# Optimization experiments

Hardware: AMD Instinct MI355X
Metric: run time of the kernel (lower is better)

The kernel has to match this reference:

```python
import jax, jax.numpy as jnp
import numpy as np
from jax import lax

B, S, T = 512, 64, 32
E, H = 512, 1024
VIN, VOUT = 128, 128


def gru_cell(x, h, W_ih, W_hh, b_ih, b_hh):
    # PyTorch GRU cell: gates ordered (r, z, n)
    gi = x @ W_ih.T + b_ih           # [B, 3*Hh]
    gh = h @ W_hh.T + b_hh           # [B, 3*Hh]
    i_r, i_z, i_n = jnp.split(gi, 3, axis=-1)
    h_r, h_z, h_n = jnp.split(gh, 3, axis=-1)
    r = jax.nn.sigmoid(i_r + h_r)
    z = jax.nn.sigmoid(i_z + h_z)
    n = jnp.tanh(i_n + r * h_n)
    return (1.0 - z) * n + z * h


def setup_inputs() -> dict:
    key = jax.random.key(0)
    ks = jax.random.split(key, 18)
    g = lambda k, shp: (jax.random.normal(k, shp, jnp.float32) * 0.05)
    return {
        "src": jax.random.randint(ks[0], (B, S), 0, VIN),
        "tgt": jax.random.randint(ks[1], (B, T), 0, VOUT),
        "enc_emb": g(ks[2], (VIN, E)),
        "dec_emb": g(ks[3], (VOUT, E)),
        "W_ih_f": g(ks[4], (3 * H, E)), "W_hh_f": g(ks[5], (3 * H, H)),
        "b_ih_f": g(ks[6], (3 * H,)), "b_hh_f": g(ks[7], (3 * H,)),
        "W_ih_b": g(ks[8], (3 * H, E)), "W_hh_b": g(ks[9], (3 * H, H)),
        "b_ih_b": g(ks[10], (3 * H,)), "b_hh_b": g(ks[11], (3 * H,)),
        "W_ih_d": g(ks[12], (3 * 2 * H, E)), "W_hh_d": g(ks[13], (3 * 2 * H, 2 * H)),
        "b_ih_d": g(ks[14], (3 * 2 * H,)), "b_hh_d": g(ks[15], (3 * 2 * H,)),
        "W_fc": g(ks[16], (VOUT, 2 * H)), "b_fc": g(ks[17], (VOUT,)),
    }


def reference(src, tgt, enc_emb, dec_emb,
              W_ih_f, W_hh_f, b_ih_f, b_hh_f,
              W_ih_b, W_hh_b, b_ih_b, b_hh_b,
              W_ih_d, W_hh_d, b_ih_d, b_hh_d,
              W_fc, b_fc):
    batch = src.shape[0]
    x = enc_emb[src]                         # [B, S, E]
    x_t = jnp.swapaxes(x, 0, 1)              # [S, B, E]

    def enc_scan(xs, W_ih, W_hh, b_ih, b_hh):
        h0 = jnp.zeros((batch, H), dtype=xs.dtype)
        def step(h, xt):
            h2 = gru_cell(xt, h, W_ih, W_hh, b_ih, b_hh)
            return h2, None
        hT, _ = lax.scan(step, h0, xs)
        return hT                             # final hidden [B, H]

    h_fwd = enc_scan(x_t, W_ih_f, W_hh_f, b_ih_f, b_hh_f)
    h_bwd = enc_scan(x_t[::-1], W_ih_b, W_hh_b, b_ih_b, b_hh_b)
    h = jnp.concatenate([h_fwd, h_bwd], axis=-1)   # [B, 2H] = torch.cat((h[-2], h[-1]), 1)

    tok0 = tgt[:, 0]                          # <sos> tokens

    def dec_step(carry, _):
        hh, tok = carry
        xt = dec_emb[tok]                     # [B, E]
        hh = gru_cell(xt, hh, W_ih_d, W_hh_d, b_ih_d, b_hh_d)
        logits = hh @ W_fc.T + b_fc           # [B, VOUT]
        nxt = jnp.argmax(logits, axis=-1)     # greedy feedback (teacher_forcing_ratio=0)
        return (hh, nxt), logits

    (_, _), logits = lax.scan(dec_step, (h, tok0), None, length=tgt.shape[1] - 1)
    return jnp.swapaxes(logits, 0, 1)         # [B, T-1, VOUT]
```

## Files before the change

### kernel.cpp

```cpp
#include <hip/hip_runtime.h>
#include <math.h>

#define B 512
#define S 64
#define T 32
#define E 512
#define H 1024
#define VOUTD 128
#define H2 (2*H)
#define H3 (3*H)
#define H6 (6*H)

typedef unsigned short ushortT;
typedef unsigned int uintT;
typedef __attribute__((ext_vector_type(8))) short short8;
typedef __attribute__((ext_vector_type(4))) float floatx4;

__device__ __forceinline__ float sigmoidf_(float x) { return 1.0f / (1.0f + expf(-x)); }

__device__ __forceinline__ uintT pack_hi2(float a, float b) {
    return (__float_as_uint(a) >> 16) | (__float_as_uint(b) & 0xFFFF0000u);
}
__device__ __forceinline__ uintT pack_lo2(float a, float b) {
    uintT ua = __float_as_uint(a), ub = __float_as_uint(b);
    uintT la = __float_as_uint(a - __uint_as_float(ua & 0xFFFF0000u)) >> 16;
    uintT lb = __float_as_uint(b - __uint_as_float(ub & 0xFFFF0000u)) >> 16;
    return la | (lb << 16);
}

__global__ __launch_bounds__(256) void zero16(uint4* __restrict__ p, int n)
{
    int i = blockIdx.x * 256 + threadIdx.x;
    if (i < n) p[i] = make_uint4(0u, 0u, 0u, 0u);
}

__global__ __launch_bounds__(256) void swizzle_w(
    const float* __restrict__ W, ushortT* __restrict__ out, int njShift, int kShift)
{
    int idx = blockIdx.x * 256 + threadIdx.x;
    int total = 3 << (njShift + kShift);
    if (idx >= total) return;
    int wrow = idx >> kShift;
    int k8 = idx & ((1 << kShift) - 1);
    int k = k8 << 3;
    int K = 8 << kShift;
    const float* s = W + (size_t)wrow * K + k;
    float4 f0 = *(const float4*)s;
    float4 f1 = *(const float4*)(s + 4);
    int g = wrow >> njShift;
    int j = wrow & ((1 << njShift) - 1);
    int jb = j >> 4, jl = j & 15;
    int c = k >> 5, kq = (k >> 3) & 3;
    int laneA = jl + 16 * kq;
    int ncK = K >> 5;
    size_t base = (((size_t)(jb * ncK + c) * 3 + g) * 2) * 512 + (size_t)laneA * 8;
    uint4 hv = make_uint4(pack_hi2(f0.x, f0.y), pack_hi2(f0.z, f0.w),
                          pack_hi2(f1.x, f1.y), pack_hi2(f1.z, f1.w));
    uint4 lv = make_uint4(pack_lo2(f0.x, f0.y), pack_lo2(f0.z, f0.w),
                          pack_lo2(f1.x, f1.y), pack_lo2(f1.z, f1.w));
    *(uint4*)(out + base) = hv;
    *(uint4*)(out + base + 512) = lv;
}

__global__ __launch_bounds__(256) void fused_step_enc(
    const ushortT* __restrict__ Afr,
    const ushortT* __restrict__ WfrF, const ushortT* __restrict__ WfrB,
    const float* __restrict__ giTabF, const float* __restrict__ giTabB,
    const int* __restrict__ src, int s,
    const float* __restrict__ bhF, const float* __restrict__ bhB,
    float* __restrict__ h, ushortT* __restrict__ AfrOut)
{
    __shared__ ushortT sB[2][24 * 512];
    __shared__ int sTok[64];
    const int t = threadIdx.x, lane = t & 63, w = t >> 6;
    const int bid = blockIdx.x;
    const int xcd = bid & 7, q = bid >> 3;
    const int jg = xcd + 8 * (q & 3);
    const int mb = q >> 2;
    const int j0 = jg * 32, m0 = mb * 64;
    const bool bwd = (m0 >= B);
    const ushortT* Wfr = bwd ? WfrB : WfrF;
    const float* giTab = bwd ? giTabB : giTabF;
    const float* bh = bwd ? bhB : bhF;
    const int NCK = 32, NIT = 16;

    if (t < 64) {
        int b = (m0 + t) & (B - 1);
        sTok[t] = src[b * S + (bwd ? (S - 1 - s) : s)];
    }

    const int wr = w >> 1, wc = w & 1;
    const ushortT* aP = Afr + (size_t)((m0 >> 4) + wr * 2) * (NCK * 1024) + lane * 8;

    const ushortT* gWb[3];
    int lds0[3], lds1[3];
#pragma unroll
    for (int k = 0; k < 3; ++k) {
        int f = w * 3 + k;
        int jbLoc = f / 6, rem = f % 6;
        gWb[k] = Wfr + (size_t)(jg * 2 + jbLoc) * (NCK * 3072) + rem * 512 + lane * 8;
        lds0[k] = f * 512 + lane * 8;
        lds1[k] = (12 + f) * 512 + lane * 8;
    }
    const int rb0 = wc * 3072 + lane * 8;

    floatx4 acc[2][3];
#pragma unroll
    for (int mi = 0; mi < 2; ++mi)
#pragma unroll
        for (int g = 0; g < 3; ++g) acc[mi][g] = (floatx4){0.f, 0.f, 0.f, 0.f};

    uint4 st0[3], st1[3];
#pragma unroll
    for (int k = 0; k < 3; ++k) {
        st0[k] = *(const uint4*)(gWb[k]);
        st1[k] = *(const uint4*)(gWb[k] + 3072);
    }
#pragma unroll
    for (int k = 0; k < 3; ++k) {
        *(uint4*)&sB[0][lds0[k]] = st0[k];
        *(uint4*)&sB[0][lds1[k]] = st1[k];
    }
    __syncthreads();

    short8 an00 = *(const short8*)(aP);
    short8 an01 = *(const short8*)(aP + 512);
    short8 an10 = *(const short8*)(aP + NCK * 1024);
    short8 an11 = *(const short8*)(aP + NCK * 1024 + 512);

    int pb = 0;
    for (int it = 0; it < NIT; ++it) {
        if (it + 1 < NIT) {
            int cb = (it + 1) * 2;
#pragma unroll
            for (int k = 0; k < 3; ++k) {
                st0[k] = *(const uint4*)(gWb[k] + (size_t)cb * 3072);
                st1[k] = *(const uint4*)(gWb[k] + (size_t)(cb + 1) * 3072);
            }
        }
        const ushortT* bp = &sB[pb][0];
        {
            short8 a00 = an00, a01 = an01, a10 = an10, a11 = an11;
            int cn = 2 * it + 1;
            an00 = *(const short8*)(aP + (size_t)cn * 1024);
            an01 = *(const short8*)(aP + (size_t)cn * 1024 + 512);
            an10 = *(const short8*)(aP + (size_t)cn * 1024 + NCK * 1024);
            an11 = *(const short8*)(aP + (size_t)cn * 1024 + NCK * 1024 + 512);
#pragma unroll
            for (int g = 0; g < 3; ++g) {
                short8 bhf = *(const short8*)&bp[rb0 + g * 1024];
                short8 blf = *(const short8*)&bp[rb0 + g * 1024 + 512];
                acc[0][g] = __builtin_amdgcn_mfma_f32_16x16x32_bf16(a00, bhf, acc[0][g], 0, 0, 0);
                acc[0][g] = __builtin_amdgcn_mfma_f32_16x16x32_bf16(a00, blf, acc[0][g], 0, 0, 0);
                acc[0][g] = __builtin_amdgcn_mfma_f32_16x16x32_bf16(a01, bhf, acc[0][g], 0, 0, 0);
                acc[1][g] = __builtin_amdgcn_mfma_f32_16x16x32_bf16(a10, bhf, acc[1][g], 0, 0, 0);
                acc[1][g] = __builtin_amdgcn_mfma_f32_16x16x32_bf16(a10, blf, acc[1][g], 0, 0, 0);
                acc[1][g] = __builtin_amdgcn_mfma_f32_16x16x32_bf16(a11, bhf, acc[1][g], 0, 0, 0);
            }
        }
        {
            short8 a00 = an00, a01 = an01, a10 = an10, a11 = an11;
            int cn = 2 * it + 2; if (cn >= NCK) cn = NCK - 1;
            an00 = *(const short8*)(aP + (size_t)cn * 1024);
            an01 = *(const short8*)(aP + (size_t)cn * 1024 + 512);
            an10 = *(const short8*)(aP + (size_t)cn * 1024 + NCK * 1024);
            an11 = *(const short8*)(aP + (size_t)cn * 1024 + NCK * 1024 + 512);
#pragma unroll
            for (int g = 0; g < 3; ++g) {
                short8 bhf = *(const short8*)&bp[12 * 512 + rb0 + g * 1024];
                short8 blf = *(const short8*)&bp[12 * 512 + rb0 + g * 1024 + 512];
                acc[0][g] = __builtin_amdgcn_mfma_f32_16x16x32_bf16(a00, bhf, acc[0][g], 0, 0, 0);
                acc[0][g] = __builtin_amdgcn_mfma_f32_16x16x32_bf16(a00, blf, acc[0][g], 0, 0, 0);
                acc[0][g] = __builtin_amdgcn_mfma_f32_16x16x32_bf16(a01, bhf, acc[0][g], 0, 0, 0);
                acc[1][g] = __builtin_amdgcn_mfma_f32_16x16x32_bf16(a10, bhf, acc[1][g], 0, 0, 0);
                acc[1][g] = __builtin_amdgcn_mfma_f32_16x16x32_bf16(a10, blf, acc[1][g], 0, 0, 0);
                acc[1][g] = __builtin_amdgcn_mfma_f32_16x16x32_bf16(a11, bhf, acc[1][g], 0, 0, 0);
            }
        }
        if (it + 1 < NIT) {
#pragma unroll
            for (int k = 0; k < 3; ++k) {
                *(uint4*)&sB[pb ^ 1][lds0[k]] = st0[k];
                *(uint4*)&sB[pb ^ 1][lds1[k]] = st1[k];
            }
            __syncthreads();
            pb ^= 1;
        }
    }

    const int colj = j0 + wc * 16 + (lane & 15);
    const float bR = bh[colj], bZ = bh[H + colj], bN = bh[2 * H + colj];
    const int rloc0 = wr * 32 + (lane >> 4) * 4;
    const int cA = colj >> 5;
    const int kqA = (colj >> 3) & 3;
    const int eA = colj & 7;
#pragma unroll
    for (int mi = 0; mi < 2; ++mi) {
#pragma unroll
        for (int r = 0; r < 4; ++r) {
            const int rloc = rloc0 + mi * 16 + r;
            const int row = m0 + rloc;
            const float* gi = giTab + (size_t)sTok[rloc] * H3;
            float ghr = acc[mi][0][r] + bR;
            float ghz = acc[mi][1][r] + bZ;
            float ghn = acc[mi][2][r] + bN;
            float rr = sigmoidf_(gi[colj] + ghr);
            float z  = sigmoidf_(gi[H + colj] + ghz);
            float n  = tanhf(gi[2 * H + colj] + rr * ghn);
            const size_t idx = (size_t)row * H + colj;
            float hnew = (1.0f - z) * n + z * h[idx];
            h[idx] = hnew;
            uintT u = __float_as_uint(hnew);
            size_t ao = (((size_t)(row >> 4) * 32 + cA) * 2) * 512
                      + (size_t)((row & 15) + 16 * kqA) * 8 + eA;
            AfrOut[ao] = (ushortT)(u >> 16);
            AfrOut[ao + 512] = (ushortT)(__float_as_uint(hnew - __uint_as_float(u & 0xFFFF0000u)) >> 16);
        }
    }
}

__global__ __launch_bounds__(256) void fused_step_dec(
    const ushortT* __restrict__ Afr, const ushortT* __restrict__ Wfr,
    const float* __restrict__ giTabD, const int* __restrict__ tok,
    const float* __restrict__ bhD,
    float* __restrict__ h, ushortT* __restrict__ AfrOut)
{
    __shared__ ushortT sB[2][24 * 512];
    __shared__ int sTok[64];
    const int t = threadIdx.x, lane = t & 63, w = t >> 6;
    const int bid = blockIdx.x;
    const int xcd = bid & 7, q = bid >> 3;
    const int jg = xcd + 8 * (q & 7);
    const int mb = q >> 3;
    const int j0 = jg * 32, m0 = mb * 64;
    const int NCK = 64, NIT = 32;

    if (t < 64) sTok[t] = tok[m0 + t];

    const int wr = w >> 1, wc = w & 1;
    const ushortT* aP = Afr + (size_t)((m0 >> 4) + wr * 2) * (NCK * 1024) + lane * 8;

    const ushortT* gWb[3];
    int lds0[3], lds1[3];
#pragma unroll
    for (int k = 0; k < 3; ++k) {
        int f = w * 3 + k;
        int jbLoc = f / 6, rem = f % 6;
        gWb[k] = Wfr + (size_t)(jg * 2 + jbLoc) * (NCK * 3072) + rem * 512 + lane * 8;
        lds0[k] = f * 512 + lane * 8;
        lds1[k] = (12 + f) * 512 + lane * 8;
    }
    const int rb0 = wc * 3072 + lane * 8;

    floatx4 acc[2][3];
#pragma unroll
    for (int mi = 0; mi < 2; ++mi)
#pragma unroll
        for (int g = 0; g < 3; ++g) acc[mi][g] = (floatx4){0.f, 0.f, 0.f, 0.f};

    uint4 st0[3], st1[3];
#pragma unroll
    for (int k = 0; k < 3; ++k) {
        st0[k] = *(const uint4*)(gWb[k]);
        st1[k] = *(const uint4*)(gWb[k] + 3072);
    }
#pragma unroll
    for (int k = 0; k < 3; ++k) {
        *(uint4*)&sB[0][lds0[k]] = st0[k];
        *(uint4*)&sB[0][lds1[k]] = st1[k];
    }
    __syncthreads();

    short8 an00 = *(const short8*)(aP);
    short8 an01 = *(const short8*)(aP + 512);
    short8 an10 = *(const short8*)(aP + NCK * 1024);
    short8 an11 = *(const short8*)(aP + NCK * 1024 + 512);

    int pb = 0;
    for (int it = 0; it < NIT; ++it) {
        if (it + 1 < NIT) {
            int cb = (it + 1) * 2;
#pragma unroll
            for (int k = 0; k < 3; ++k) {
                st0[k] = *(const uint4*)(gWb[k] + (size_t)cb * 3072);
                st1[k] = *(const uint4*)(gWb[k] + (size_t)(cb + 1) * 3072);
            }
        }
        const ushortT* bp = &sB[pb][0];
        {
            short8 a00 = an00, a01 = an01, a10 = an10, a11 = an11;
            int cn = 2 * it + 1;
            an00 = *(const short8*)(aP + (size_t)cn * 1024);
            an01 = *(const short8*)(aP + (size_t)cn * 1024 + 512);
            an10 = *(const short8*)(aP + (size_t)cn * 1024 + NCK * 1024);
            an11 = *(const short8*)(aP + (size_t)cn * 1024 + NCK * 1024 + 512);
#pragma unroll
            for (int g = 0; g < 3; ++g) {
                short8 bhf = *(const short8*)&bp[rb0 + g * 1024];
                short8 blf = *(const short8*)&bp[rb0 + g * 1024 + 512];
                acc[0][g] = __builtin_amdgcn_mfma_f32_16x16x32_bf16(a00, bhf, acc[0][g], 0, 0, 0);
                acc[0][g] = __builtin_amdgcn_mfma_f32_16x16x32_bf16(a00, blf, acc[0][g], 0, 0, 0);
                acc[0][g] = __builtin_amdgcn_mfma_f32_16x16x32_bf16(a01, bhf, acc[0][g], 0, 0, 0);
                acc[1][g] = __builtin_amdgcn_mfma_f32_16x16x32_bf16(a10, bhf, acc[1][g], 0, 0, 0);
                acc[1][g] = __builtin_amdgcn_mfma_f32_16x16x32_bf16(a10, blf, acc[1][g], 0, 0, 0);
                acc[1][g] = __builtin_amdgcn_mfma_f32_16x16x32_bf16(a11, bhf, acc[1][g], 0, 0, 0);
            }
        }
        {
            short8 a00 = an00, a01 = an01, a10 = an10, a11 = an11;
            int cn = 2 * it + 2; if (cn >= NCK) cn = NCK - 1;
            an00 = *(const short8*)(aP + (size_t)cn * 1024);
            an01 = *(const short8*)(aP + (size_t)cn * 1024 + 512);
            an10 = *(const short8*)(aP + (size_t)cn * 1024 + NCK * 1024);
            an11 = *(const short8*)(aP + (size_t)cn * 1024 + NCK * 1024 + 512);
#pragma unroll
            for (int g = 0; g < 3; ++g) {
                short8 bhf = *(const short8*)&bp[12 * 512 + rb0 + g * 1024];
                short8 blf = *(const short8*)&bp[12 * 512 + rb0 + g * 1024 + 512];
                acc[0][g] = __builtin_amdgcn_mfma_f32_16x16x32_bf16(a00, bhf, acc[0][g], 0, 0, 0);
                acc[0][g] = __builtin_amdgcn_mfma_f32_16x16x32_bf16(a00, blf, acc[0][g], 0, 0, 0);
                acc[0][g] = __builtin_amdgcn_mfma_f32_16x16x32_bf16(a01, bhf, acc[0][g], 0, 0, 0);
                acc[1][g] = __builtin_amdgcn_mfma_f32_16x16x32_bf16(a10, bhf, acc[1][g], 0, 0, 0);
                acc[1][g] = __builtin_amdgcn_mfma_f32_16x16x32_bf16(a10, blf, acc[1][g], 0, 0, 0);
                acc[1][g] = __builtin_amdgcn_mfma_f32_16x16x32_bf16(a11, bhf, acc[1][g], 0, 0, 0);
            }
        }
        if (it + 1 < NIT) {
#pragma unroll
            for (int k = 0; k < 3; ++k) {
                *(uint4*)&sB[pb ^ 1][lds0[k]] = st0[k];
                *(uint4*)&sB[pb ^ 1][lds1[k]] = st1[k];
            }
            __syncthreads();
            pb ^= 1;
        }
    }

    const int colj = j0 + wc * 16 + (lane & 15);
    const float bR = bhD[colj], bZ = bhD[H2 + colj], bN = bhD[2 * H2 + colj];
    const int rloc0 = wr * 32 + (lane >> 4) * 4;
    const int cA = colj >> 5;
    const int kqA = (colj >> 3) & 3;
    const int eA = colj & 7;
#pragma unroll
    for (int mi = 0; mi < 2; ++mi) {
#pragma unroll
        for (int r = 0; r < 4; ++r) {
            const int rloc = rloc0 + mi * 16 + r;
            const int row = m0 + rloc;
            const float* gi = giTabD + (size_t)sTok[rloc] * H6;
            float ghr = acc[mi][0][r] + bR;
            float ghz = acc[mi][1][r] + bZ;
            float ghn = acc[mi][2][r] + bN;
            float rr = sigmoidf_(gi[colj] + ghr);
            float z  = sigmoidf_(gi[H2 + colj] + ghz);
            float n  = tanhf(gi[2 * H2 + colj] + rr * ghn);
            const size_t idx = (size_t)row * H2 + colj;
            float hnew = (1.0f - z) * n + z * h[idx];
            h[idx] = hnew;
            uintT u = __float_as_uint(hnew);
            size_t ao = (((size_t)(row >> 4) * 64 + cA) * 2) * 512
                      + (size_t)((row & 15) + 16 * kqA) * 8 + eA;
            AfrOut[ao] = (ushortT)(u >> 16);
            AfrOut[ao + 512] = (ushortT)(__float_as_uint(hnew - __uint_as_float(u & 0xFFFF0000u)) >> 16);
        }
    }
}

__global__ __launch_bounds__(256) void init_hh_tok_split(
    const float* __restrict__ h_f, const float* __restrict__ h_b,
    const int* __restrict__ tgt, float* __restrict__ hh,
    ushortT* __restrict__ AfrD, int* __restrict__ tok)
{
    int i = blockIdx.x * blockDim.x + threadIdx.x;
    int b = i >> 11;
    int j = i & 2047;
    float v = (j < H) ? h_f[(size_t)b * H + j] : h_b[(size_t)b * H + (j - H)];
    hh[i] = v;
    uintT u = __float_as_uint(v);
    size_t ao = (((size_t)(b >> 4) * 64 + (j >> 5)) * 2) * 512
              + (size_t)((b & 15) + 16 * ((j >> 3) & 3)) * 8 + (j & 7);
    AfrD[ao] = (ushortT)(u >> 16);
    AfrD[ao + 512] = (ushortT)(__float_as_uint(v - __uint_as_float(u & 0xFFFF0000u)) >> 16);
    if (j == 0) tok[b] = tgt[b * T];
}

__global__ __launch_bounds__(256) void logits_argmax2(
    const float* __restrict__ hh, const float* __restrict__ W_fc,
    const float* __restrict__ b_fc, float* __restrict__ out,
    int* __restrict__ tok, int t)
{
    __shared__ float sh[2][H2];
    __shared__ float sred[2][2][128];
    __shared__ float sval[2][128];
    __shared__ int   sidx[2][128];
    const int tid = threadIdx.x;
    const int col = tid & 127;
    const int kh  = tid >> 7;
    const int b0  = blockIdx.x * 2;

    {
        const float4* srcp = (const float4*)(hh + (size_t)b0 * H2);
        float4* dst = (float4*)sh;
        for (int i = tid; i < 2 * H2 / 4; i += 256) dst[i] = srcp[i];
    }
    __syncthreads();

    const float* wrow = W_fc + (size_t)col * H2 + kh * (H2 / 2);
    const float* s0 = sh[0] + kh * (H2 / 2);
    const float* s1 = sh[1] + kh * (H2 / 2);
    float a0 = 0.f, a1 = 0.f;
#pragma unroll 8
    for (int k = 0; k < H2 / 2; k += 4) {
        float4 w4 = *(const float4*)(wrow + k);
        float4 h0 = *(const float4*)(s0 + k);
        float4 h1 = *(const float4*)(s1 + k);
        a0 += w4.x * h0.x + w4.y * h0.y + w4.z * h0.z + w4.w * h0.w;
        a1 += w4.x * h1.x + w4.y * h1.y + w4.z * h1.z + w4.w * h1.w;
    }
    sred[kh][0][col] = a0;
    sred[kh][1][col] = a1;
    __syncthreads();

    if (kh == 0) {
        float l0 = sred[0][0][col] + sred[1][0][col] + b_fc[col];
        float l1 = sred[0][1][col] + sred[1][1][col] + b_fc[col];
        out[(size_t)(b0 + 0) * ((T - 1) * VOUTD) + (size_t)t * VOUTD + col] = l0;
        out[(size_t)(b0 + 1) * ((T - 1) * VOUTD) + (size_t)t * VOUTD + col] = l1;
        sval[0][col] = l0; sidx[0][col] = col;
        sval[1][col] = l1; sidx[1][col] = col;
    }
    __syncthreads();

    const int r = tid >> 7, c = tid & 127;
    for (int off = 64; off > 0; off >>= 1) {
        if (c < off) {
            float ov = sval[r][c + off]; int oi = sidx[r][c + off];
            if (ov > sval[r][c] || (ov == sval[r][c] && oi < sidx[r][c])) {
                sval[r][c] = ov; sidx[r][c] = oi;
            }
        }
        __syncthreads();
    }
    if (tid < 2) tok[b0 + tid] = sidx[tid][0];
}

__global__ __launch_bounds__(256) void gemm_bias(
    const float* __restrict__ Abase,
    const int* __restrict__ idx, int idxStride, int idxOff, int lda,
    const float* __restrict__ W, const float* __restrict__ bias,
    float* __restrict__ C, int N, int K)
{
    __shared__ float As[16][68];
    __shared__ float Ws[16][68];
    const int t = threadIdx.x;
    const int m0 = blockIdx.y * 64, n0 = blockIdx.x * 64;
    const int lr = t >> 2, lc = (t & 3) << 2;
    const int tx = t & 15, ty = t >> 4;
    const int tn0 = tx << 2, tm0 = ty << 2;
    const int arow = m0 + lr;
    const float* Aptr = idx ? (Abase + (size_t)idx[arow * idxStride + idxOff] * lda)
                            : (Abase + (size_t)arow * lda);
    const float* Wptr = W + (size_t)(n0 + lr) * K;
    float acc[4][4] = {{0.f}};
    for (int k0 = 0; k0 < K; k0 += 16) {
        float4 a4 = *(const float4*)(Aptr + k0 + lc);
        float4 w4 = *(const float4*)(Wptr + k0 + lc);
        __syncthreads();
        As[lc+0][lr] = a4.x; As[lc+1][lr] = a4.y; As[lc+2][lr] = a4.z; As[lc+3][lr] = a4.w;
        Ws[lc+0][lr] = w4.x; Ws[lc+1][lr] = w4.y; Ws[lc+2][lr] = w4.z; Ws[lc+3][lr] = w4.w;
        __syncthreads();
#pragma unroll
        for (int kk = 0; kk < 16; ++kk) {
            float4 av = *(const float4*)&As[kk][tm0];
            float4 wv = *(const float4*)&Ws[kk][tn0];
            float am[4] = {av.x, av.y, av.z, av.w};
            float wn[4] = {wv.x, wv.y, wv.z, wv.w};
#pragma unroll
            for (int i = 0; i < 4; ++i)
#pragma unroll
                for (int j = 0; j < 4; ++j) acc[i][j] += am[i] * wn[j];
        }
    }
    const float b0 = bias[n0+tn0], b1 = bias[n0+tn0+1], b2 = bias[n0+tn0+2], b3 = bias[n0+tn0+3];
#pragma unroll
    for (int i = 0; i < 4; ++i) {
        float4 o = make_float4(acc[i][0]+b0, acc[i][1]+b1, acc[i][2]+b2, acc[i][3]+b3);
        *(float4*)(C + (size_t)(m0 + tm0 + i) * N + n0 + tn0) = o;
    }
}

__global__ __launch_bounds__(256) void gemm_enc(
    const float* __restrict__ Abase, int lda, int K,
    const int* __restrict__ srcIdx, int s,
    const float* __restrict__ W1, const float* __restrict__ bias1,
    const float* __restrict__ W2, const float* __restrict__ bias2,
    float* __restrict__ C, int N)
{
    __shared__ float As[16][68];
    __shared__ float Ws[16][68];
    const int t = threadIdx.x;
    const int m0 = blockIdx.y * 64, n0 = blockIdx.x * 64;
    const bool bwd = (m0 >= B);
    const float* W = bwd ? W2 : W1;
    const float* bias = bwd ? bias2 : bias1;
    const int lr = t >> 2, lc = (t & 3) << 2;
    const int tx = t & 15, ty = t >> 4;
    const int tn0 = tx << 2, tm0 = ty << 2;
    const int arow = m0 + lr;
    const float* Aptr;
    if (srcIdx) {
        int r = arow & (B - 1);
        int sidx = bwd ? (S - 1 - s) : s;
        Aptr = Abase + (size_t)srcIdx[r * S + sidx] * lda;
    } else Aptr = Abase + (size_t)arow * lda;
    const float* Wptr = W + (size_t)(n0 + lr) * K;
    float acc[4][4] = {{0.f}};
    for (int k0 = 0; k0 < K; k0 += 16) {
        float4 a4 = *(const float4*)(Aptr + k0 + lc);
        float4 w4 = *(const float4*)(Wptr + k0 + lc);
        __syncthreads();
        As[lc+0][lr] = a4.x; As[lc+1][lr] = a4.y; As[lc+2][lr] = a4.z; As[lc+3][lr] = a4.w;
        Ws[lc+0][lr] = w4.x; Ws[lc+1][lr] = w4.y; Ws[lc+2][lr] = w4.z; Ws[lc+3][lr] = w4.w;
        __syncthreads();
#pragma unroll
        for (int kk = 0; kk < 16; ++kk) {
            float4 av = *(const float4*)&As[kk][tm0];
            float4 wv = *(const float4*)&Ws[kk][tn0];
            float am[4] = {av.x, av.y, av.z, av.w};
            float wn[4] = {wv.x, wv.y, wv.z, wv.w};
#pragma unroll
            for (int i = 0; i < 4; ++i)
#pragma unroll
                for (int j = 0; j < 4; ++j) acc[i][j] += am[i] * wn[j];
        }
    }
    const float b0 = bias[n0+tn0], b1 = bias[n0+tn0+1], b2 = bias[n0+tn0+2], b3 = bias[n0+tn0+3];
#pragma unroll
    for (int i = 0; i < 4; ++i) {
        float4 o = make_float4(acc[i][0]+b0, acc[i][1]+b1, acc[i][2]+b2, acc[i][3]+b3);
        *(float4*)(C + (size_t)(m0 + tm0 + i) * N + n0 + tn0) = o;
    }
}

__global__ __launch_bounds__(256) void gru_gate(
    const float* __restrict__ gi, const float* __restrict__ gh,
    float* __restrict__ h, int Hd)
{
    int i = blockIdx.x * blockDim.x + threadIdx.x;
    int b = i / Hd, j = i - b * Hd;
    const float* gib = gi + (size_t)b * 3 * Hd;
    const float* ghb = gh + (size_t)b * 3 * Hd;
    float r = sigmoidf_(gib[j] + ghb[j]);
    float z = sigmoidf_(gib[Hd + j] + ghb[Hd + j]);
    float n = tanhf(gib[2 * Hd + j] + r * ghb[2 * Hd + j]);
    h[i] = (1.0f - z) * n + z * h[i];
}

__global__ __launch_bounds__(256) void init_hh_tok(
    const float* __restrict__ h_f, const float* __restrict__ h_b,
    const int* __restrict__ tgt, float* __restrict__ hh, int* __restrict__ tok)
{
    int i = blockIdx.x * blockDim.x + threadIdx.x;
    int b = i >> 11, j = i & 2047;
    hh[i] = (j < H) ? h_f[(size_t)b * H + j] : h_b[(size_t)b * H + (j - H)];
    if (j == 0) tok[b] = tgt[b * T];
}

extern "C" void kernel_launch(void* const* d_in, const int* in_sizes, int n_in,
                              void* d_out, int out_size, void* d_ws, size_t ws_size,
                              hipStream_t stream)
{
    const int*   src     = (const int*)d_in[0];
    const int*   tgt     = (const int*)d_in[1];
    const float* enc_emb = (const float*)d_in[2];
    const float* dec_emb = (const float*)d_in[3];
    const float* W_ih_f  = (const float*)d_in[4];
    const float* W_hh_f  = (const float*)d_in[5];
    const float* b_ih_f  = (const float*)d_in[6];
    const float* b_hh_f  = (const float*)d_in[7];
    const float* W_ih_b  = (const float*)d_in[8];
    const float* W_hh_b  = (const float*)d_in[9];
    const float* b_ih_b  = (const float*)d_in[10];
    const float* b_hh_b  = (const float*)d_in[11];
    const float* W_ih_d  = (const float*)d_in[12];
    const float* W_hh_d  = (const float*)d_in[13];
    const float* b_ih_d  = (const float*)d_in[14];
    const float* b_hh_d  = (const float*)d_in[15];
    const float* W_fc    = (const float*)d_in[16];
    const float* b_fc    = (const float*)d_in[17];
    float* out = (float*)d_out;

    char* base = (char*)d_ws;
    size_t off = 0;
    auto alloc = [&](size_t bytes) { char* p = base + off; off += (bytes + 255) & ~(size_t)255; return p; };

    float*   hE     = (float*)  alloc((size_t)2 * B * H * 4);
    ushortT* AfrEA  = (ushortT*)alloc((size_t)2 * B * H * 2 * 2);
    ushortT* AfrEB  = (ushortT*)alloc((size_t)2 * B * H * 2 * 2);
    float*   hh     = (float*)  alloc((size_t)B * H2 * 4);
    ushortT* AfrDA  = (ushortT*)alloc((size_t)B * H2 * 2 * 2);
    ushortT* AfrDB  = (ushortT*)alloc((size_t)B * H2 * 2 * 2);
    float*   giTabF = (float*)  alloc((size_t)VOUTD * H3 * 4);
    float*   giTabB = (float*)  alloc((size_t)VOUTD * H3 * 4);
    float*   giTabD = (float*)  alloc((size_t)VOUTD * H6 * 4);
    ushortT* WfrF   = (ushortT*)alloc((size_t)H3 * H * 2 * 2);
    ushortT* WfrB   = (ushortT*)alloc((size_t)H3 * H * 2 * 2);
    ushortT* WfrD   = (ushortT*)alloc((size_t)H6 * H2 * 2 * 2);
    int*     tok    = (int*)    alloc((size_t)B * 4);
    size_t required = off;

    dim3 blk(256);

    if (ws_size >= required) {
        {
            size_t zbytes = (size_t)2 * B * H * 4 + (size_t)2 * B * H * 4;
            int n16 = (int)(zbytes / 16);
            zero16<<<dim3((n16 + 255) / 256), blk, 0, stream>>>((uint4*)hE, n16);
        }
        swizzle_w<<<dim3((3 * H3 * H / (3 * 8) * 3 / 256) ? ((3 << 17) + 255) / 256 : 1), blk, 0, stream>>>(
            W_hh_f, WfrF, 10, 7);
        swizzle_w<<<dim3(((3 << 17) + 255) / 256), blk, 0, stream>>>(W_hh_b, WfrB, 10, 7);
        swizzle_w<<<dim3(((3 << 19) + 255) / 256), blk, 0, stream>>>(W_hh_d, WfrD, 11, 8);

        gemm_bias<<<dim3(H3 / 64, VOUTD / 64), blk, 0, stream>>>(
            enc_emb, nullptr, 0, 0, E, W_ih_f, b_ih_f, giTabF, H3, E);
        gemm_bias<<<dim3(H3 / 64, VOUTD / 64), blk, 0, stream>>>(
            enc_emb, nullptr, 0, 0, E, W_ih_b, b_ih_b, giTabB, H3, E);
        gemm_bias<<<dim3(H6 / 64, VOUTD / 64), blk, 0, stream>>>(
            dec_emb, nullptr, 0, 0, E, W_ih_d, b_ih_d, giTabD, H6, E);

        for (int s = 0; s < S; ++s) {
            const ushortT* inA = (s & 1) ? AfrEB : AfrEA;
            ushortT* outA = (s & 1) ? AfrEA : AfrEB;
            fused_step_enc<<<dim3(512), blk, 0, stream>>>(
                inA, WfrF, WfrB, giTabF, giTabB, src, s, b_hh_f, b_hh_b, hE, outA);
        }

        init_hh_tok_split<<<dim3((B * H2) / 256), blk, 0, stream>>>(
            hE, hE + (size_t)B * H, tgt, hh, AfrDA, tok);

        for (int t = 0; t < T - 1; ++t) {
            const ushortT* inA = (t & 1) ? AfrDB : AfrDA;
            ushortT* outA = (t & 1) ? AfrDA : AfrDB;
            fused_step_dec<<<dim3(512), blk, 0, stream>>>(
                inA, WfrD, giTabD, tok, b_hh_d, hh, outA);
            logits_argmax2<<<dim3(B / 2), blk, 0, stream>>>(hh, W_fc, b_fc, out, tok, t);
        }
    } else {
        {
            size_t zbytes = (size_t)2 * B * H * 4;
            int n16 = (int)(zbytes / 16);
            zero16<<<dim3((n16 + 255) / 256), blk, 0, stream>>>((uint4*)hE, n16);
        }
        float* giE = (float*)WfrF;
        float* ghF = giE + (size_t)2 * B * H3;
        dim3 grid_gi(H3 / 64, (2 * B) / 64);
        dim3 grid_gate((2 * B * H) / 256);
        for (int s = 0; s < S; ++s) {
            gemm_enc<<<grid_gi, blk, 0, stream>>>(enc_emb, E, E, src, s,
                                                  W_ih_f, b_ih_f, W_ih_b, b_ih_b, giE, H3);
            gemm_enc<<<grid_gi, blk, 0, stream>>>(hE, H, H, nullptr, 0,
                                                  W_hh_f, b_hh_f, W_hh_b, b_hh_b, ghF, H3);
            gru_gate<<<grid_gate, blk, 0, stream>>>(giE, ghF, hE, H);
        }
        init_hh_tok<<<dim3((B * H2) / 256), blk, 0, stream>>>(hE, hE + (size_t)B * H, tgt, hh, tok);
        dim3 grid_d(H6 / 64, B / 64);
        dim3 grid_dgate((B * H2) / 256);
        for (int t = 0; t < T - 1; ++t) {
            gemm_bias<<<grid_d, blk, 0, stream>>>(dec_emb, tok, 1, 0, E,
                                                  W_ih_d, b_ih_d, giE, H6, E);
            gemm_bias<<<grid_d, blk, 0, stream>>>(hh, nullptr, 0, 0, H2,
                                                  W_hh_d, b_hh_d, ghF, H6, H2);
            gru_gate<<<grid_dgate, blk, 0, stream>>>(giE, ghF, hh, H2);
            logits_argmax2<<<dim3(B / 2), blk, 0, stream>>>(hh, W_fc, b_fc, out, tok, t);
        }
    }
}
```

Baseline: 4.854 ms.

## Deepen GRU step prefetch pipeline, coalesce weight swizzle, split-K embedding gate GEMMs

The encoder and decoder recurrent step kernels now prefetch weight chunks two stages ahead in registers and load A fragments a full pair of chunks ahead, using macro-unrolled ping-pong buffers with a single barrier per pair. The weight swizzle kernel is reorganised so each wavefront writes one contiguous fragment, making stores coalesced. The small embedding-table input-gate GEMMs use a 4-way split-K kernel plus a combine pass to get more parallelism. Holding more prefetched fragments raises register pressure, which may lower occupancy.

```diff
diff --git a/kernel.cpp b/kernel.cpp
--- a/kernel.cpp
+++ b/kernel.cpp
@@ -37,30 +37,78 @@
 __global__ __launch_bounds__(256) void swizzle_w(
     const float* __restrict__ W, ushortT* __restrict__ out, int njShift, int kShift)
 {
-    int idx = blockIdx.x * 256 + threadIdx.x;
-    int total = 3 << (njShift + kShift);
-    if (idx >= total) return;
-    int wrow = idx >> kShift;
-    int k8 = idx & ((1 << kShift) - 1);
-    int k = k8 << 3;
-    int K = 8 << kShift;
-    const float* s = W + (size_t)wrow * K + k;
+    const int K = 8 << kShift;
+    const int nj = 1 << njShift;
+    const int ncK = K >> 5;
+    const int total = (nj >> 4) * ncK * 3;
+    int f = blockIdx.x * 4 + (threadIdx.x >> 6);
+    if (f >= total) return;
+    const int lane = threadIdx.x & 63;
+    int g = f % 3;
+    int rest = f / 3;
+    int c = rest & (ncK - 1);
+    int jb = rest >> (kShift - 2);
+    int jl = lane & 15, kq = lane >> 4;
+    int row = g * nj + jb * 16 + jl;
+    int k = c * 32 + kq * 8;
+    const float* s = W + (size_t)row * K + k;
     float4 f0 = *(const float4*)s;
     float4 f1 = *(const float4*)(s + 4);
-    int g = wrow >> njShift;
-    int j = wrow & ((1 << njShift) - 1);
-    int jb = j >> 4, jl = j & 15;
-    int c = k >> 5, kq = (k >> 3) & 3;
-    int laneA = jl + 16 * kq;
-    int ncK = K >> 5;
-    size_t base = (((size_t)(jb * ncK + c) * 3 + g) * 2) * 512 + (size_t)laneA * 8;
     uint4 hv = make_uint4(pack_hi2(f0.x, f0.y), pack_hi2(f0.z, f0.w),
                           pack_hi2(f1.x, f1.y), pack_hi2(f1.z, f1.w));
     uint4 lv = make_uint4(pack_lo2(f0.x, f0.y), pack_lo2(f0.z, f0.w),
                           pack_lo2(f1.x, f1.y), pack_lo2(f1.z, f1.w));
+    size_t base = (size_t)f * 1024 + (size_t)lane * 8;
     *(uint4*)(out + base) = hv;
     *(uint4*)(out + base + 512) = lv;
 }
+
+#define MFMA16(a, b, c) __builtin_amdgcn_mfma_f32_16x16x32_bf16(a, b, c, 0, 0, 0)
+
+#define CHUNK_MFMA(PB, CLOC, ACUR)                                              \
+    {                                                                           \
+        const ushortT* bp = &sB[PB][(CLOC) * 12 * 512];                         \
+        _Pragma("unroll")                                                       \
+        for (int g = 0; g < 3; ++g) {                                           \
+            short8 bhf = *(const short8*)&bp[rb0 + g * 1024];                   \
+            short8 blf = *(const short8*)&bp[rb0 + g * 1024 + 512];             \
+            acc[0][g] = MFMA16(ACUR[(CLOC)*4+0], bhf, acc[0][g]);               \
+            acc[0][g] = MFMA16(ACUR[(CLOC)*4+0], blf, acc[0][g]);               \
+            acc[0][g] = MFMA16(ACUR[(CLOC)*4+1], bhf, acc[0][g]);               \
+            acc[1][g] = MFMA16(ACUR[(CLOC)*4+2], bhf, acc[1][g]);               \
+            acc[1][g] = MFMA16(ACUR[(CLOC)*4+2], blf, acc[1][g]);               \
+            acc[1][g] = MFMA16(ACUR[(CLOC)*4+3], bhf, acc[1][g]);               \
+        }                                                                       \
+    }
+
+#define PAIR_BODY(IP, ACUR, BRDY, ANXT, BFLY, PB)                               \
+    {                                                                           \
+        if ((IP) + 2 < NP) {                                                    \
+            _Pragma("unroll")                                                   \
+            for (int k = 0; k < 3; ++k) {                                       \
+                BFLY[k]     = *(const uint4*)(gWb[k] + (size_t)(2*(IP)+4) * 3072); \
+                BFLY[3 + k] = *(const uint4*)(gWb[k] + (size_t)(2*(IP)+5) * 3072); \
+            }                                                                   \
+        }                                                                       \
+        if ((IP) + 1 < NP) {                                                    \
+            _Pragma("unroll")                                                   \
+            for (int c = 0; c < 2; ++c) {                                       \
+                const ushortT* ap_ = aP + (size_t)(2*(IP)+2 + c) * 1024;        \
+                ANXT[c*4+0] = *(const short8*)(ap_);                            \
+                ANXT[c*4+1] = *(const short8*)(ap_ + 512);                      \
+                ANXT[c*4+2] = *(const short8*)(ap_ + NCKd * 1024);              \
+                ANXT[c*4+3] = *(const short8*)(ap_ + NCKd * 1024 + 512);        \
+            }                                                                   \
+            _Pragma("unroll")                                                   \
+            for (int k = 0; k < 3; ++k) {                                       \
+                *(uint4*)&sB[(PB) ^ 1][lds0[k]] = BRDY[k];                      \
+                *(uint4*)&sB[(PB) ^ 1][lds1[k]] = BRDY[3 + k];                  \
+            }                                                                   \
+        }                                                                       \
+        CHUNK_MFMA(PB, 0, ACUR);                                                \
+        CHUNK_MFMA(PB, 1, ACUR);                                                \
+        __syncthreads();                                                        \
+    }
 
 __global__ __launch_bounds__(256) void fused_step_enc(
     const ushortT* __restrict__ Afr,
@@ -82,7 +130,7 @@
     const ushortT* Wfr = bwd ? WfrB : WfrF;
     const float* giTab = bwd ? giTabB : giTabF;
     const float* bh = bwd ? bhB : bhF;
-    const int NCK = 32, NIT = 16;
+    const int NCKd = 32, NP = 16;
 
     if (t < 64) {
         int b = (m0 + t) & (B - 1);
@@ -90,7 +138,7 @@
     }
 
     const int wr = w >> 1, wc = w & 1;
-    const ushortT* aP = Afr + (size_t)((m0 >> 4) + wr * 2) * (NCK * 1024) + lane * 8;
+    const ushortT* aP = Afr + (size_t)((m0 >> 4) + wr * 2) * (NCKd * 1024) + lane * 8;
 
     const ushortT* gWb[3];
     int lds0[3], lds1[3];
@@ -98,7 +146,7 @@
     for (int k = 0; k < 3; ++k) {
         int f = w * 3 + k;
         int jbLoc = f / 6, rem = f % 6;
-        gWb[k] = Wfr + (size_t)(jg * 2 + jbLoc) * (NCK * 3072) + rem * 512 + lane * 8;
+        gWb[k] = Wfr + (size_t)(jg * 2 + jbLoc) * (NCKd * 3072) + rem * 512 + lane * 8;
         lds0[k] = f * 512 + lane * 8;
         lds1[k] = (12 + f) * 512 + lane * 8;
     }
@@ -110,82 +158,40 @@
 #pragma unroll
         for (int g = 0; g < 3; ++g) acc[mi][g] = (floatx4){0.f, 0.f, 0.f, 0.f};
 
-    uint4 st0[3], st1[3];
-#pragma unroll
-    for (int k = 0; k < 3; ++k) {
-        st0[k] = *(const uint4*)(gWb[k]);
-        st1[k] = *(const uint4*)(gWb[k] + 3072);
-    }
-#pragma unroll
-    for (int k = 0; k < 3; ++k) {
-        *(uint4*)&sB[0][lds0[k]] = st0[k];
-        *(uint4*)&sB[0][lds1[k]] = st1[k];
+    short8 aA[8], aB[8];
+    uint4 bA[6], bB[6];
+
+    {
+        uint4 p0[6];
+#pragma unroll
+        for (int k = 0; k < 3; ++k) {
+            p0[k]     = *(const uint4*)(gWb[k]);
+            p0[3 + k] = *(const uint4*)(gWb[k] + 3072);
+        }
+#pragma unroll
+        for (int c = 0; c < 2; ++c) {
+            const ushortT* ap_ = aP + (size_t)c * 1024;
+            aA[c*4+0] = *(const short8*)(ap_);
+            aA[c*4+1] = *(const short8*)(ap_ + 512);
+            aA[c*4+2] = *(const short8*)(ap_ + NCKd * 1024);
+            aA[c*4+3] = *(const short8*)(ap_ + NCKd * 1024 + 512);
+        }
+#pragma unroll
+        for (int k = 0; k < 3; ++k) {
+            bA[k]     = *(const uint4*)(gWb[k] + 2 * 3072);
+            bA[3 + k] = *(const uint4*)(gWb[k] + 3 * 3072);
+        }
+#pragma unroll
+        for (int k = 0; k < 3; ++k) {
+            *(uint4*)&sB[0][lds0[k]] = p0[k];
+            *(uint4*)&sB[0][lds1[k]] = p0[3 + k];
+        }
     }
     __syncthreads();
 
-    short8 an00 = *(const short8*)(aP);
-    short8 an01 = *(const short8*)(aP + 512);
-    short8 an10 = *(const short8*)(aP + NCK * 1024);
-    short8 an11 = *(const short8*)(aP + NCK * 1024 + 512);
-
-    int pb = 0;
-    for (int it = 0; it < NIT; ++it) {
-        if (it + 1 < NIT) {
-            int cb = (it + 1) * 2;
-#pragma unroll
-            for (int k = 0; k < 3; ++k) {
-                st0[k] = *(const uint4*)(gWb[k] + (size_t)cb * 3072);
-                st1[k] = *(const uint4*)(gWb[k] + (size_t)(cb + 1) * 3072);
-            }
-        }
-        const ushortT* bp = &sB[pb][0];
-        {
-            short8 a00 = an00, a01 = an01, a10 = an10, a11 = an11;
-            int cn = 2 * it + 1;
-            an00 = *(const short8*)(aP + (size_t)cn * 1024);
-            an01 = *(const short8*)(aP + (size_t)cn * 1024 + 512);
-            an10 = *(const short8*)(aP + (size_t)cn * 1024 + NCK * 1024);
-            an11 = *(const short8*)(aP + (size_t)cn * 1024 + NCK * 1024 + 512);
-#pragma unroll
-            for (int g = 0; g < 3; ++g) {
-                short8 bhf = *(const short8*)&bp[rb0 + g * 1024];
-                short8 blf = *(const short8*)&bp[rb0 + g * 1024 + 512];
-                acc[0][g] = __builtin_amdgcn_mfma_f32_16x16x32_bf16(a00, bhf, acc[0][g], 0, 0, 0);
-                acc[0][g] = __builtin_amdgcn_mfma_f32_16x16x32_bf16(a00, blf, acc[0][g], 0, 0, 0);
-                acc[0][g] = __builtin_amdgcn_mfma_f32_16x16x32_bf16(a01, bhf, acc[0][g], 0, 0, 0);
-                acc[1][g] = __builtin_amdgcn_mfma_f32_16x16x32_bf16(a10, bhf, acc[1][g], 0, 0, 0);
-                acc[1][g] = __builtin_amdgcn_mfma_f32_16x16x32_bf16(a10, blf, acc[1][g], 0, 0, 0);
-                acc[1][g] = __builtin_amdgcn_mfma_f32_16x16x32_bf16(a11, bhf, acc[1][g], 0, 0, 0);
-            }
-        }
-        {
-            short8 a00 = an00, a01 = an01, a10 = an10, a11 = an11;
-            int cn = 2 * it + 2; if (cn >= NCK) cn = NCK - 1;
-            an00 = *(const short8*)(aP + (size_t)cn * 1024);
-            an01 = *(const short8*)(aP + (size_t)cn * 1024 + 512);
-            an10 = *(const short8*)(aP + (size_t)cn * 1024 + NCK * 1024);
-            an11 = *(const short8*)(aP + (size_t)cn * 1024 + NCK * 1024 + 512);
-#pragma unroll
-            for (int g = 0; g < 3; ++g) {
-                short8 bhf = *(const short8*)&bp[12 * 512 + rb0 + g * 1024];
-                short8 blf = *(const short8*)&bp[12 * 512 + rb0 + g * 1024 + 512];
-                acc[0][g] = __builtin_amdgcn_mfma_f32_16x16x32_bf16(a00, bhf, acc[0][g], 0, 0, 0);
-                acc[0][g] = __builtin_amdgcn_mfma_f32_16x16x32_bf16(a00, blf, acc[0][g], 0, 0, 0);
-                acc[0][g] = __builtin_amdgcn_mfma_f32_16x16x32_bf16(a01, bhf, acc[0][g], 0, 0, 0);
-                acc[1][g] = __builtin_amdgcn_mfma_f32_16x16x32_bf16(a10, bhf, acc[1][g], 0, 0, 0);
-                acc[1][g] = __builtin_amdgcn_mfma_f32_16x16x32_bf16(a10, blf, acc[1][g], 0, 0, 0);
-                acc[1][g] = __builtin_amdgcn_mfma_f32_16x16x32_bf16(a11, bhf, acc[1][g], 0, 0, 0);
-            }
-        }
-        if (it + 1 < NIT) {
-#pragma unroll
-            for (int k = 0; k < 3; ++k) {
-                *(uint4*)&sB[pb ^ 1][lds0[k]] = st0[k];
-                *(uint4*)&sB[pb ^ 1][lds1[k]] = st1[k];
-            }
-            __syncthreads();
-            pb ^= 1;
-        }
+    for (int ip = 0; ip < NP; ip += 2) {
+        PAIR_BODY(ip,     aA, bA, aB, bB, 0);
+        PAIR_BODY(ip + 1, aB, bB, aA, bA, 1);
     }
 
     const int colj = j0 + wc * 16 + (lane & 15);
@@ -233,12 +239,12 @@
     const int jg = xcd + 8 * (q & 7);
     const int mb = q >> 3;
     const int j0 = jg * 32, m0 = mb * 64;
-    const int NCK = 64, NIT = 32;
+    const int NCKd = 64, NP = 32;
 
     if (t < 64) sTok[t] = tok[m0 + t];
 
     const int wr = w >> 1, wc = w & 1;
-    const ushortT* aP = Afr + (size_t)((m0 >> 4) + wr * 2) * (NCK * 1024) + lane * 8;
+    const ushortT* aP = Afr + (size_t)((m0 >> 4) + wr * 2) * (NCKd * 1024) + lane * 8;
 
     const ushortT* gWb[3];
     int lds0[3], lds1[3];
@@ -246,7 +252,7 @@
     for (int k = 0; k < 3; ++k) {
         int f = w * 3 + k;
         int jbLoc = f / 6, rem = f % 6;
-        gWb[k] = Wfr + (size_t)(jg * 2 + jbLoc) * (NCK * 3072) + rem * 512 + lane * 8;
+        gWb[k] = Wfr + (size_t)(jg * 2 + jbLoc) * (NCKd * 3072) + rem * 512 + lane * 8;
         lds0[k] = f * 512 + lane * 8;
         lds1[k] = (12 + f) * 512 + lane * 8;
     }
@@ -258,82 +264,40 @@
 #pragma unroll
         for (int g = 0; g < 3; ++g) acc[mi][g] = (floatx4){0.f, 0.f, 0.f, 0.f};
 
-    uint4 st0[3], st1[3];
-#pragma unroll
-    for (int k = 0; k < 3; ++k) {
-        st0[k] = *(const uint4*)(gWb[k]);
-        st1[k] = *(const uint4*)(gWb[k] + 3072);
-    }
-#pragma unroll
-    for (int k = 0; k < 3; ++k) {
-        *(uint4*)&sB[0][lds0[k]] = st0[k];
-        *(uint4*)&sB[0][lds1[k]] = st1[k];
+    short8 aA[8], aB[8];
+    uint4 bA[6], bB[6];
+
+    {
+        uint4 p0[6];
+#pragma unroll
+        for (int k = 0; k < 3; ++k) {
+            p0[k]     = *(const uint4*)(gWb[k]);
+            p0[3 + k] = *(const uint4*)(gWb[k] + 3072);
+        }
+#pragma unroll
+        for (int c = 0; c < 2; ++c) {
+            const ushortT* ap_ = aP + (size_t)c * 1024;
+            aA[c*4+0] = *(const short8*)(ap_);
+            aA[c*4+1] = *(const short8*)(ap_ + 512);
+            aA[c*4+2] = *(const short8*)(ap_ + NCKd * 1024);
+            aA[c*4+3] = *(const short8*)(ap_ + NCKd * 1024 + 512);
+        }
+#pragma unroll
+        for (int k = 0; k < 3; ++k) {
+            bA[k]     = *(const uint4*)(gWb[k] + 2 * 3072);
+            bA[3 + k] = *(const uint4*)(gWb[k] + 3 * 3072);
+        }
+#pragma unroll
+        for (int k = 0; k < 3; ++k) {
+            *(uint4*)&sB[0][lds0[k]] = p0[k];
+            *(uint4*)&sB[0][lds1[k]] = p0[3 + k];
+        }
     }
     __syncthreads();
 
-    short8 an00 = *(const short8*)(aP);
-    short8 an01 = *(const short8*)(aP + 512);
-    short8 an10 = *(const short8*)(aP + NCK * 1024);
-    short8 an11 = *(const short8*)(aP + NCK * 1024 + 512);
-
-    int pb = 0;
-    for (int it = 0; it < NIT; ++it) {
-        if (it + 1 < NIT) {
-            int cb = (it + 1) * 2;
-#pragma unroll
-            for (int k = 0; k < 3; ++k) {
-                st0[k] = *(const uint4*)(gWb[k] + (size_t)cb * 3072);
-                st1[k] = *(const uint4*)(gWb[k] + (size_t)(cb + 1) * 3072);
-            }
-        }
-        const ushortT* bp = &sB[pb][0];
-        {
-            short8 a00 = an00, a01 = an01, a10 = an10, a11 = an11;
-            int cn = 2 * it + 1;
-            an00 = *(const short8*)(aP + (size_t)cn * 1024);
-            an01 = *(const short8*)(aP + (size_t)cn * 1024 + 512);
-            an10 = *(const short8*)(aP + (size_t)cn * 1024 + NCK * 1024);
-            an11 = *(const short8*)(aP + (size_t)cn * 1024 + NCK * 1024 + 512);
-#pragma unroll
-            for (int g = 0; g < 3; ++g) {
-                short8 bhf = *(const short8*)&bp[rb0 + g * 1024];
-                short8 blf = *(const short8*)&bp[rb0 + g * 1024 + 512];
-                acc[0][g] = __builtin_amdgcn_mfma_f32_16x16x32_bf16(a00, bhf, acc[0][g], 0, 0, 0);
-                acc[0][g] = __builtin_amdgcn_mfma_f32_16x16x32_bf16(a00, blf, acc[0][g], 0, 0, 0);
-                acc[0][g] = __builtin_amdgcn_mfma_f32_16x16x32_bf16(a01, bhf, acc[0][g], 0, 0, 0);
-                acc[1][g] = __builtin_amdgcn_mfma_f32_16x16x32_bf16(a10, bhf, acc[1][g], 0, 0, 0);
-                acc[1][g] = __builtin_amdgcn_mfma_f32_16x16x32_bf16(a10, blf, acc[1][g], 0, 0, 0);
-                acc[1][g] = __builtin_amdgcn_mfma_f32_16x16x32_bf16(a11, bhf, acc[1][g], 0, 0, 0);
-            }
-        }
-        {
-            short8 a00 = an00, a01 = an01, a10 = an10, a11 = an11;
-            int cn = 2 * it + 2; if (cn >= NCK) cn = NCK - 1;
-            an00 = *(const short8*)(aP + (size_t)cn * 1024);
-            an01 = *(const short8*)(aP + (size_t)cn * 1024 + 512);
-            an10 = *(const short8*)(aP + (size_t)cn * 1024 + NCK * 1024);
-            an11 = *(const short8*)(aP + (size_t)cn * 1024 + NCK * 1024 + 512);
-#pragma unroll
-            for (int g = 0; g < 3; ++g) {
-                short8 bhf = *(const short8*)&bp[12 * 512 + rb0 + g * 1024];
-                short8 blf = *(const short8*)&bp[12 * 512 + rb0 + g * 1024 + 512];
-                acc[0][g] = __builtin_amdgcn_mfma_f32_16x16x32_bf16(a00, bhf, acc[0][g], 0, 0, 0);
-                acc[0][g] = __builtin_amdgcn_mfma_f32_16x16x32_bf16(a00, blf, acc[0][g], 0, 0, 0);
-                acc[0][g] = __builtin_amdgcn_mfma_f32_16x16x32_bf16(a01, bhf, acc[0][g], 0, 0, 0);
-                acc[1][g] = __builtin_amdgcn_mfma_f32_16x16x32_bf16(a10, bhf, acc[1][g], 0, 0, 0);
-                acc[1][g] = __builtin_amdgcn_mfma_f32_16x16x32_bf16(a10, blf, acc[1][g], 0, 0, 0);
-                acc[1][g] = __builtin_amdgcn_mfma_f32_16x16x32_bf16(a11, bhf, acc[1][g], 0, 0, 0);
-            }
-        }
-        if (it + 1 < NIT) {
-#pragma unroll
-            for (int k = 0; k < 3; ++k) {
-                *(uint4*)&sB[pb ^ 1][lds0[k]] = st0[k];
-                *(uint4*)&sB[pb ^ 1][lds1[k]] = st1[k];
-            }
-            __syncthreads();
-            pb ^= 1;
-        }
+    for (int ip = 0; ip < NP; ip += 2) {
+        PAIR_BODY(ip,     aA, bA, aB, bB, 0);
+        PAIR_BODY(ip + 1, aB, bB, aA, bA, 1);
     }
 
     const int colj = j0 + wc * 16 + (lane & 15);
@@ -443,6 +407,57 @@
         __syncthreads();
     }
     if (tid < 2) tok[b0 + tid] = sidx[tid][0];
+}
+
+__global__ __launch_bounds__(256) void gemm_sk(
+    const float* __restrict__ Abase, int lda,
+    const float* __restrict__ W, float* __restrict__ Cp, int N, int K, int KS)
+{
+    __shared__ float As[16][68];
+    __shared__ float Ws[16][68];
+    const int t = threadIdx.x;
+    const int m0 = blockIdx.y * 64, n0 = blockIdx.x * 64;
+    const int Kc = K / KS, kb = blockIdx.z * Kc;
+    const int lr = t >> 2, lc = (t & 3) << 2;
+    const int tx = t & 15, ty = t >> 4;
+    const int tn0 = tx << 2, tm0 = ty << 2;
+    const float* Aptr = Abase + (size_t)(m0 + lr) * lda + kb;
+    const float* Wptr = W + (size_t)(n0 + lr) * K + kb;
+    float acc[4][4] = {{0.f}};
+    for (int k0 = 0; k0 < Kc; k0 += 16) {
+        float4 a4 = *(const float4*)(Aptr + k0 + lc);
+        float4 w4 = *(const float4*)(Wptr + k0 + lc);
+        __syncthreads();
+        As[lc+0][lr] = a4.x; As[lc+1][lr] = a4.y; As[lc+2][lr] = a4.z; As[lc+3][lr] = a4.w;
+        Ws[lc+0][lr] = w4.x; Ws[lc+1][lr] = w4.y; Ws[lc+2][lr] = w4.z; Ws[lc+3][lr] = w4.w;
+        __syncthreads();
+#pragma unroll
+        for (int kk = 0; kk < 16; ++kk) {
+            float4 av = *(const float4*)&As[kk][tm0];
+            float4 wv = *(const float4*)&Ws[kk][tn0];
+            float am[4] = {av.x, av.y, av.z, av.w};
+            float wn[4] = {wv.x, wv.y, wv.z, wv.w};
+#pragma unroll
+            for (int i = 0; i < 4; ++i)
+#pragma unroll
+                for (int j = 0; j < 4; ++j) acc[i][j] += am[i] * wn[j];
+        }
+    }
+    float* Cb = Cp + ((size_t)blockIdx.z * VOUTD + m0 + tm0) * N + n0 + tn0;
+#pragma unroll
+    for (int i = 0; i < 4; ++i)
+        *(float4*)(Cb + (size_t)i * N) = make_float4(acc[i][0], acc[i][1], acc[i][2], acc[i][3]);
+}
+
+__global__ __launch_bounds__(256) void gi_combine(
+    const float* __restrict__ Cp, const float* __restrict__ bias,
+    float* __restrict__ Cout, int N, int KS)
+{
+    int j = blockIdx.x * 256 + threadIdx.x;
+    int v = blockIdx.y;
+    float s = 0.f;
+    for (int z = 0; z < KS; ++z) s += Cp[((size_t)z * VOUTD + v) * N + j];
+    Cout[(size_t)v * N + j] = s + bias[j];
 }
 
 __global__ __launch_bounds__(256) void gemm_bias(
@@ -604,6 +619,7 @@
     float*   giTabF = (float*)  alloc((size_t)VOUTD * H3 * 4);
     float*   giTabB = (float*)  alloc((size_t)VOUTD * H3 * 4);
     float*   giTabD = (float*)  alloc((size_t)VOUTD * H6 * 4);
+    float*   giPart = (float*)  alloc((size_t)4 * VOUTD * H6 * 4);
     ushortT* WfrF   = (ushortT*)alloc((size_t)H3 * H * 2 * 2);
     ushortT* WfrB   = (ushortT*)alloc((size_t)H3 * H * 2 * 2);
     ushortT* WfrD   = (ushortT*)alloc((size_t)H6 * H2 * 2 * 2);
@@ -618,17 +634,23 @@
             int n16 = (int)(zbytes / 16);
             zero16<<<dim3((n16 + 255) / 256), blk, 0, stream>>>((uint4*)hE, n16);
         }
-        swizzle_w<<<dim3((3 * H3 * H / (3 * 8) * 3 / 256) ? ((3 << 17) + 255) / 256 : 1), blk, 0, stream>>>(
-            W_hh_f, WfrF, 10, 7);
-        swizzle_w<<<dim3(((3 << 17) + 255) / 256), blk, 0, stream>>>(W_hh_b, WfrB, 10, 7);
-        swizzle_w<<<dim3(((3 << 19) + 255) / 256), blk, 0, stream>>>(W_hh_d, WfrD, 11, 8);
-
-        gemm_bias<<<dim3(H3 / 64, VOUTD / 64), blk, 0, stream>>>(
-            enc_emb, nullptr, 0, 0, E, W_ih_f, b_ih_f, giTabF, H3, E);
-        gemm_bias<<<dim3(H3 / 64, VOUTD / 64), blk, 0, stream>>>(
-            enc_emb, nullptr, 0, 0, E, W_ih_b, b_ih_b, giTabB, H3, E);
-        gemm_bias<<<dim3(H6 / 64, VOUTD / 64), blk, 0, stream>>>(
-            dec_emb, nullptr, 0, 0, E, W_ih_d, b_ih_d, giTabD, H6, E);
+        {
+            int fe = (H / 16) * (H / 32) * 3;
+            int fd = (H2 / 16) * (H2 / 32) * 3;
+            swizzle_w<<<dim3((fe + 3) / 4), blk, 0, stream>>>(W_hh_f, WfrF, 10, 7);
+            swizzle_w<<<dim3((fe + 3) / 4), blk, 0, stream>>>(W_hh_b, WfrB, 10, 7);
+            swizzle_w<<<dim3((fd + 3) / 4), blk, 0, stream>>>(W_hh_d, WfrD, 11, 8);
+        }
+
+        gemm_sk<<<dim3(H3 / 64, VOUTD / 64, 4), blk, 0, stream>>>(
+            enc_emb, E, W_ih_f, giPart, H3, E, 4);
+        gi_combine<<<dim3(H3 / 256, VOUTD), blk, 0, stream>>>(giPart, b_ih_f, giTabF, H3, 4);
+        gemm_sk<<<dim3(H3 / 64, VOUTD / 64, 4), blk, 0, stream>>>(
+            enc_emb, E, W_ih_b, giPart, H3, E, 4);
+        gi_combine<<<dim3(H3 / 256, VOUTD), blk, 0, stream>>>(giPart, b_ih_b, giTabB, H3, 4);
+        gemm_sk<<<dim3(H6 / 64, VOUTD / 64, 4), blk, 0, stream>>>(
+            dec_emb, E, W_ih_d, giPart, H6, E, 4);
+        gi_combine<<<dim3(H6 / 256, VOUTD), blk, 0, stream>>>(giPart, b_ih_d, giTabD, H6, 4);
 
         for (int s = 0; s < S; ++s) {
             const ushortT* inA = (s & 1) ? AfrEB : AfrEA;
```

After: 9.844 ms. 103% more time.
